# Kernel tuning notes

Hardware: AMD Instinct MI355X
Metric: run time of the kernel (lower is better)

The kernel has to match this reference:

```python
import jax, jax.numpy as jnp
import numpy as np

HEADS = 48
HEAD_DIM = 64
DIM = 3072
RANK = 128
TEXT_LEN = 226
VID_LEN = 1822
B = 1
LORA_W = 1.0
EPS = 1e-5


def setup_inputs() -> dict:
    key = jax.random.key(0)
    ks = jax.random.split(key, 24)
    s = 0.02  # weight init scale
    inp = {
        "hidden_states": jax.random.normal(ks[0], (B, VID_LEN, DIM), jnp.float32),
        "encoder_hidden_states": jax.random.normal(ks[1], (B, TEXT_LEN, DIM), jnp.float32),
        "rope_cos": jax.random.uniform(ks[2], (VID_LEN, HEAD_DIM), jnp.float32),
        "rope_sin": jax.random.uniform(ks[3], (VID_LEN, HEAD_DIM), jnp.float32),
        "Wq": jax.random.normal(ks[4], (DIM, DIM), jnp.float32) * s,
        "bq": jax.random.normal(ks[5], (DIM,), jnp.float32) * s,
        "Wk": jax.random.normal(ks[6], (DIM, DIM), jnp.float32) * s,
        "bk": jax.random.normal(ks[7], (DIM,), jnp.float32) * s,
        "Wv": jax.random.normal(ks[8], (DIM, DIM), jnp.float32) * s,
        "bv": jax.random.normal(ks[9], (DIM,), jnp.float32) * s,
        "Wo": jax.random.normal(ks[10], (DIM, DIM), jnp.float32) * s,
        "bo": jax.random.normal(ks[11], (DIM,), jnp.float32) * s,
        "lq_down": jax.random.normal(ks[12], (RANK, DIM), jnp.float32) / RANK,
        "lq_up": jax.random.normal(ks[13], (DIM, RANK), jnp.float32) * s,
        "lk_down": jax.random.normal(ks[14], (RANK, DIM), jnp.float32) / RANK,
        "lk_up": jax.random.normal(ks[15], (DIM, RANK), jnp.float32) * s,
        "lv_down": jax.random.normal(ks[16], (RANK, DIM), jnp.float32) / RANK,
        "lv_up": jax.random.normal(ks[17], (DIM, RANK), jnp.float32) * s,
        "lp_down": jax.random.normal(ks[18], (RANK, DIM), jnp.float32) / RANK,
        "lp_up": jax.random.normal(ks[19], (DIM, RANK), jnp.float32) * s,
        "gamma_q": jnp.ones((HEAD_DIM,), jnp.float32),
        "beta_q": jnp.zeros((HEAD_DIM,), jnp.float32),
        "gamma_k": jnp.ones((HEAD_DIM,), jnp.float32),
        "beta_k": jnp.zeros((HEAD_DIM,), jnp.float32),
    }
    return inp


def _lora(x, down, up):
    # x: [B,S,DIM]; down: [RANK,DIM]; up: [DIM,RANK]
    return (x @ down.T) @ up.T


def _layernorm(x, gamma, beta):
    mu = jnp.mean(x, axis=-1, keepdims=True)
    var = jnp.mean(jnp.square(x - mu), axis=-1, keepdims=True)
    return (x - mu) * jax.lax.rsqrt(var + EPS) * gamma + beta


def _apply_rope(x, cos, sin):
    # diffusers apply_rotary_emb, use_real=True, unbind_dim=-1
    # x: [B,H,S,D]; cos/sin: [S,D]
    xr = x.reshape(*x.shape[:-1], HEAD_DIM // 2, 2)
    x1, x2 = xr[..., 0], xr[..., 1]
    x_rot = jnp.stack([-x2, x1], axis=-1).reshape(x.shape)
    return x * cos + x_rot * sin


def reference(hidden_states, encoder_hidden_states, rope_cos, rope_sin,
              Wq, bq, Wk, bk, Wv, bv, Wo, bo,
              lq_down, lq_up, lk_down, lk_up, lv_down, lv_up, lp_down, lp_up,
              gamma_q, beta_q, gamma_k, beta_k):
    h = jnp.concatenate([encoder_hidden_states, hidden_states], axis=1)  # [B,S,DIM]
    S = h.shape[1]

    q = h @ Wq.T + bq + _lora(h, lq_down, lq_up) * LORA_W
    k = h @ Wk.T + bk + _lora(h, lk_down, lk_up) * LORA_W
    v = h @ Wv.T + bv + _lora(h, lv_down, lv_up) * LORA_W

    def split_heads(x):  # [B,S,DIM] -> [B,H,S,D]
        return x.reshape(B, S, HEADS, HEAD_DIM).transpose(0, 2, 1, 3)

    q, k, v = split_heads(q), split_heads(k), split_heads(v)
    q = _layernorm(q, gamma_q, beta_q)
    k = _layernorm(k, gamma_k, beta_k)

    # RoPE on video tokens only
    q = q.at[:, :, TEXT_LEN:].set(_apply_rope(q[:, :, TEXT_LEN:], rope_cos, rope_sin))
    k = k.at[:, :, TEXT_LEN:].set(_apply_rope(k[:, :, TEXT_LEN:], rope_cos, rope_sin))

    # scaled dot-product attention (no mask, no dropout)
    scale = 1.0 / np.sqrt(HEAD_DIM).astype(np.float32)
    scores = jnp.einsum("bhqd,bhkd->bhqk", q, k) * scale
    probs = jax.nn.softmax(scores, axis=-1)
    attn_out = jnp.einsum("bhqk,bhkd->bhqd", probs, v)

    out = attn_out.transpose(0, 2, 1, 3).reshape(B, S, DIM)
    out = out @ Wo.T + bo + _lora(out, lp_down, lp_up) * LORA_W

    enc_out = out[:, :TEXT_LEN, :]
    hid_out = out[:, TEXT_LEN:, :]
    return (hid_out, enc_out)
```

## Files before the change

kernel.cpp:

```cpp
#include <hip/hip_runtime.h>
#include <hip/hip_bf16.h>
#include <stdint.h>

#define S_TOT 2048
#define TEXT 226
#define VID 1822
#define DIM 3072
#define NH 48
#define HD 64

typedef __bf16 bf16x8 __attribute__((ext_vector_type(8)));
typedef __bf16 bf16x4 __attribute__((ext_vector_type(4)));
typedef float f32x4 __attribute__((ext_vector_type(4)));

#define AS1 __attribute__((address_space(1)))
#define AS3 __attribute__((address_space(3)))

__device__ __forceinline__ void g2l16(const void* g, void* l) {
    __builtin_amdgcn_global_load_lds((const AS1 uint32_t*)(uintptr_t)g,
                                     (AS3 uint32_t*)(uintptr_t)l, 16, 0, 0);
}

__device__ __forceinline__ f32x4 mfma16(bf16x4 a, bf16x4 b, f32x4 c) {
#if __has_builtin(__builtin_amdgcn_mfma_f32_16x16x16bf16_1k)
    typedef short s4 __attribute__((ext_vector_type(4)));
    union U { bf16x4 b; s4 s; };
    U ua, ub; ua.b = a; ub.b = b;
    return __builtin_amdgcn_mfma_f32_16x16x16bf16_1k(ua.s, ub.s, c, 0, 0, 0);
#else
    f32x4 d = c;
    asm volatile("v_mfma_f32_16x16x16_bf16 %0, %1, %2, %0"
                 : "+v"(d) : "v"(a), "v"(b));
    return d;
#endif
}

#define ARENA_N 47431680ull

struct NormArgs { const void* p[24]; };

__global__ __launch_bounds__(256)
void normalize_inputs(NormArgs a, __bf16* __restrict__ arena)
{
    static constexpr unsigned long long segStart[25] = {
        0ull, 694272ull, 6291456ull, 15728640ull, 25165824ull, 34603008ull,
        44040192ull, 44433408ull, 44826624ull, 45219840ull, 45613056ull,
        46006272ull, 46399488ull, 46792704ull, 47185920ull, 47302528ull,
        47419136ull, 47422208ull, 47425280ull, 47428352ull, 47431424ull,
        47431488ull, 47431552ull, 47431616ull, 47431680ull };
    static constexpr int segIn[24] = {
        1, 0, 4, 6, 8, 10, 12, 13, 14, 15, 16, 17, 18, 19, 2, 3,
        5, 7, 9, 11, 20, 21, 22, 23 };

    const uint32_t w0 = *(const uint32_t*)a.p[20];
    const bool f32in = (w0 == 0x3F800000u);

    const size_t i0 = ((size_t)blockIdx.x * 256 + threadIdx.x) * 8;
    if (i0 >= ARENA_N) return;
    int s = 0;
    while (i0 >= segStart[s + 1]) s++;
    const size_t off = i0 - segStart[s];

    if (f32in) {
        const float* src = (const float*)a.p[segIn[s]] + off;
        const float4 v0 = ((const float4*)src)[0];
        const float4 v1 = ((const float4*)src)[1];
        bf16x8 o;
        o[0] = (__bf16)v0.x; o[1] = (__bf16)v0.y; o[2] = (__bf16)v0.z; o[3] = (__bf16)v0.w;
        o[4] = (__bf16)v1.x; o[5] = (__bf16)v1.y; o[6] = (__bf16)v1.z; o[7] = (__bf16)v1.w;
        *(bf16x8*)(arena + i0) = o;
    } else {
        const __bf16* src = (const __bf16*)a.p[segIn[s]] + off;
        *(uint4*)(arena + i0) = *(const uint4*)src;
    }
}

__device__ __forceinline__ void mm_chunks(
    const __bf16* __restrict__ Ag, int lda, const __bf16* __restrict__ Bg, int ldb,
    int kbeg, int kend, f32x4 (&acc)[4][4], __bf16* As, __bf16* Bs,
    int wave, int srow, int l15, int quad, int wm, int wn)
{
    for (int k0 = kbeg; k0 < kend; k0 += 32) {
        __syncthreads();
#pragma unroll
        for (int i = 0; i < 2; i++) {
            const int blk = i * 4 + wave;
            const int r = blk * 16 + srow;
            g2l16(Ag + (size_t)r * lda + k0, &As[blk * 512]);
            g2l16(Bg + (size_t)r * ldb + k0, &Bs[blk * 512]);
        }
        __syncthreads();
        bf16x8 af[4], bfr[4];
#pragma unroll
        for (int i = 0; i < 4; i++)
            af[i] = *(const bf16x8*)&As[(wm + i * 16 + l15) * 32 + quad * 8];
#pragma unroll
        for (int j = 0; j < 4; j++)
            bfr[j] = *(const bf16x8*)&Bs[(wn + j * 16 + l15) * 32 + quad * 8];
#pragma unroll
        for (int i = 0; i < 4; i++)
#pragma unroll
            for (int j = 0; j < 4; j++)
                acc[i][j] = __builtin_amdgcn_mfma_f32_16x16x32_bf16(af[i], bfr[j], acc[i][j], 0, 0, 0);
    }
}

template<bool ATOMIC, bool FUSE2, bool TO_OUT>
__global__ __launch_bounds__(256)
void gemm_bt(const __bf16* __restrict__ A, int lda,
             const __bf16* __restrict__ B0, const __bf16* __restrict__ B1,
             const __bf16* __restrict__ B2, int ldb,
             const __bf16* __restrict__ bias0, const __bf16* __restrict__ bias1,
             const __bf16* __restrict__ bias2,
             const __bf16* __restrict__ A2, int lda2, int a2ColOff,
             const __bf16* __restrict__ U0, const __bf16* __restrict__ U1,
             const __bf16* __restrict__ U2, int ldu,
             float* __restrict__ C, int ldc,
             int K, int K2, int tilesPerGroup, int kChunk,
             void* __restrict__ dout, const void* __restrict__ probe)
{
    __shared__ __bf16 As[128 * 32];
    __shared__ __bf16 Bs[128 * 32];
    const int tid  = threadIdx.x;
    const int wave = tid >> 6;
    const int lane = tid & 63;
    const int l15  = lane & 15, quad = lane >> 4;
    const int bm = blockIdx.x, bn = blockIdx.y;
    const int group = bn / tilesPerGroup;
    const int nt    = bn - group * tilesPerGroup;
    const __bf16* B    = (group == 0) ? B0 : ((group == 1) ? B1 : B2);
    const __bf16* bias = (group == 0) ? bias0 : ((group == 1) ? bias1 : bias2);

    const int k0s = blockIdx.z * kChunk;
    int k0e = k0s + kChunk; if (k0e > K) k0e = K;

    const int srow = lane >> 2;
    const int schk = (lane & 3) * 8;
    const __bf16* Ag = A + (size_t)(bm * 128) * lda + schk;
    const __bf16* Bg = B + (size_t)(nt * 128) * ldb + schk;

    f32x4 acc[4][4] = {};
    const int wm = (wave & 1) * 64;
    const int wn = (wave >> 1) * 64;

    mm_chunks(Ag, lda, Bg, ldb, k0s, k0e, acc, As, Bs, wave, srow, l15, quad, wm, wn);

    if (FUSE2) {
        const __bf16* U = (group == 0) ? U0 : ((group == 1) ? U1 : U2);
        const __bf16* A2g = A2 + group * a2ColOff + (size_t)(bm * 128) * lda2 + schk;
        const __bf16* Ug  = U + (size_t)(nt * 128) * ldu + schk;
        mm_chunks(A2g, lda2, Ug, ldu, 0, K2, acc, As, Bs, wave, srow, l15, quad, wm, wn);
    }

    bool f32out = false;
    if (TO_OUT) f32out = (*(const uint32_t*)probe == 0x3F800000u);

#pragma unroll
    for (int i = 0; i < 4; i++) {
#pragma unroll
        for (int j = 0; j < 4; j++) {
            const int coll = wn + j * 16 + l15;
            const int col  = bn * 128 + coll;
            float bv = 0.f;
            if (bias) bv = (float)bias[nt * 128 + coll];
#pragma unroll
            for (int r = 0; r < 4; r++) {
                const int row = bm * 128 + wm + i * 16 + quad * 4 + r;
                float v = acc[i][j][r] + bv;
                if (TO_OUT) {
                    const size_t mrow = (row < TEXT) ? (size_t)(row + VID) : (size_t)(row - TEXT);
                    if (f32out) ((float*)dout)[mrow * DIM + col] = v;
                    else        ((__bf16*)dout)[mrow * DIM + col] = (__bf16)v;
                } else if (ATOMIC) {
                    atomicAdd(C + (size_t)row * ldc + col, v);
                } else {
                    C[(size_t)row * ldc + col] = v;
                }
            }
        }
    }
}

__global__ __launch_bounds__(256)
void ln_rope(const float* __restrict__ qkv,
             const __bf16* __restrict__ gq, const __bf16* __restrict__ bq,
             const __bf16* __restrict__ gk, const __bf16* __restrict__ bk,
             const __bf16* __restrict__ cosb, const __bf16* __restrict__ sinb,
             __bf16* __restrict__ qh, __bf16* __restrict__ kh)
{
    const int s = blockIdx.x;
    const int wave = threadIdx.x >> 6, lane = threadIdx.x & 63;
    for (int idx = wave; idx < 2 * NH; idx += 4) {
        const int mat  = idx / NH;
        const int head = idx - mat * NH;
        float x = qkv[(size_t)s * 9216 + mat * DIM + head * HD + lane];
        float mu = x;
        mu += __shfl_xor(mu, 1, 64);  mu += __shfl_xor(mu, 2, 64);
        mu += __shfl_xor(mu, 4, 64);  mu += __shfl_xor(mu, 8, 64);
        mu += __shfl_xor(mu, 16, 64); mu += __shfl_xor(mu, 32, 64);
        mu *= 0.015625f;
        float d = x - mu;
        float vv = d * d;
        vv += __shfl_xor(vv, 1, 64);  vv += __shfl_xor(vv, 2, 64);
        vv += __shfl_xor(vv, 4, 64);  vv += __shfl_xor(vv, 8, 64);
        vv += __shfl_xor(vv, 16, 64); vv += __shfl_xor(vv, 32, 64);
        vv *= 0.015625f;
        const float g = (float)(mat ? gk[lane] : gq[lane]);
        const float b = (float)(mat ? bk[lane] : bq[lane]);
        float y = d * rsqrtf(vv + 1e-5f) * g + b;
        if (s >= TEXT) {
            const int pos = s - TEXT;
            const float c  = (float)cosb[pos * HD + lane];
            const float sn = (float)sinb[pos * HD + lane];
            const float oth = __shfl_xor(y, 1, 64);
            const float rot = (lane & 1) ? oth : -oth;
            y = y * c + rot * sn;
        }
        __bf16* dst = mat ? kh : qh;
        dst[((size_t)head * S_TOT + s) * HD + lane] = (__bf16)y;
    }
}

__global__ __launch_bounds__(256)
void vtrans(const float* __restrict__ qkv, __bf16* __restrict__ vt)
{
    __shared__ float tile[64][65];
    const int h = blockIdx.x, sb = blockIdx.y;
    const int tid = threadIdx.x;
    const int r0 = tid >> 4;
    const int c0 = (tid & 15) * 4;
#pragma unroll
    for (int p = 0; p < 4; p++) {
        const int r = p * 16 + r0;
        const float4 v = *(const float4*)&qkv[((size_t)(sb * 64 + r)) * 9216 + 2 * DIM + h * HD + c0];
        tile[r][c0 + 0] = v.x; tile[r][c0 + 1] = v.y;
        tile[r][c0 + 2] = v.z; tile[r][c0 + 3] = v.w;
    }
    __syncthreads();
#pragma unroll
    for (int p = 0; p < 4; p++) {
        const int d = p * 16 + r0;
        __bf16 o[4];
#pragma unroll
        for (int e = 0; e < 4; e++) o[e] = (__bf16)tile[c0 + e][d];
        *(uint2*)&vt[((size_t)(h * HD + d)) * S_TOT + sb * 64 + c0] = *(const uint2*)o;
    }
}

#define KS_LD 72
#define VS_LD 136

__global__ __launch_bounds__(256)
void flash_attn(const __bf16* __restrict__ qh, const __bf16* __restrict__ kh,
                const __bf16* __restrict__ vt, __bf16* __restrict__ outp)
{
    __shared__ __bf16 Ks[128 * KS_LD];
    __shared__ __bf16 Vs[64 * VS_LD];
    const int qb = blockIdx.x, h = blockIdx.y;
    const int tid = threadIdx.x, wave = tid >> 6, lane = tid & 63;
    const int l15 = lane & 15, quad = lane >> 4;

    bf16x8 qf[2][2];
#pragma unroll
    for (int t = 0; t < 2; t++)
#pragma unroll
        for (int ks = 0; ks < 2; ks++) {
            const __bf16* p = qh + ((size_t)(h * S_TOT + qb * 128 + wave * 32 + t * 16 + l15)) * HD
                                 + ks * 32 + quad * 8;
            bf16x8 v = *(const bf16x8*)p;
#pragma unroll
            for (int e = 0; e < 8; e++) v[e] = (__bf16)((float)v[e] * 0.125f);
            qf[t][ks] = v;
        }

    f32x4 of[2][4] = {};
    float m_i[2] = {-1e30f, -1e30f};
    float l_i[2] = {0.f, 0.f};
    const float L2E = 1.44269504f;

    for (int kb = 0; kb < S_TOT / 128; kb++) {
        bf16x8 kr[4], vr[4];
#pragma unroll
        for (int p = 0; p < 4; p++) {
            const int id = p * 256 + tid;
            const int krow = id >> 3, kc = (id & 7) * 8;
            kr[p] = *(const bf16x8*)(kh + ((size_t)(h * S_TOT + kb * 128 + krow)) * HD + kc);
            const int vrow = id >> 4, vc = (id & 15) * 8;
            vr[p] = *(const bf16x8*)(vt + ((size_t)(h * HD + vrow)) * S_TOT + kb * 128 + vc);
        }
        __syncthreads();
#pragma unroll
        for (int p = 0; p < 4; p++) {
            const int id = p * 256 + tid;
            const int krow = id >> 3, kc = (id & 7) * 8;
            *(bf16x8*)&Ks[krow * KS_LD + kc] = kr[p];
            const int vrow = id >> 4, vc = (id & 15) * 8;
            *(bf16x8*)&Vs[vrow * VS_LD + vc] = vr[p];
        }
        __syncthreads();

        f32x4 sf[2][8];
#pragma unroll
        for (int n = 0; n < 8; n++) {
            const bf16x8 k0 = *(const bf16x8*)&Ks[(n * 16 + l15) * KS_LD + quad * 8];
            const bf16x8 k1 = *(const bf16x8*)&Ks[(n * 16 + l15) * KS_LD + 32 + quad * 8];
#pragma unroll
            for (int t = 0; t < 2; t++) {
                f32x4 z = {0.f, 0.f, 0.f, 0.f};
                z = __builtin_amdgcn_mfma_f32_16x16x32_bf16(k0, qf[t][0], z, 0, 0, 0);
                sf[t][n] = __builtin_amdgcn_mfma_f32_16x16x32_bf16(k1, qf[t][1], z, 0, 0, 0);
            }
        }

        float alpha_l[2];
#pragma unroll
        for (int t = 0; t < 2; t++) {
            float mx = sf[t][0][0];
#pragma unroll
            for (int n = 0; n < 8; n++)
#pragma unroll
                for (int r = 0; r < 4; r++) mx = fmaxf(mx, sf[t][n][r]);
            mx = fmaxf(mx, __shfl_xor(mx, 16, 64));
            mx = fmaxf(mx, __shfl_xor(mx, 32, 64));
            const float mnew = fmaxf(m_i[t], mx);
            alpha_l[t] = __builtin_amdgcn_exp2f((m_i[t] - mnew) * L2E);
            m_i[t] = mnew;
            float rs = 0.f;
#pragma unroll
            for (int n = 0; n < 8; n++)
#pragma unroll
                for (int r = 0; r < 4; r++) {
                    const float pv = __builtin_amdgcn_exp2f((sf[t][n][r] - mnew) * L2E);
                    sf[t][n][r] = pv;
                    rs += pv;
                }
            rs += __shfl_xor(rs, 16, 64);
            rs += __shfl_xor(rs, 32, 64);
            l_i[t] = l_i[t] * alpha_l[t] + rs;
        }

        bf16x4 pf[2][8];
#pragma unroll
        for (int t = 0; t < 2; t++)
#pragma unroll
            for (int kk = 0; kk < 8; kk++) {
                bf16x4 o;
                o[0] = (__bf16)sf[t][kk][0]; o[1] = (__bf16)sf[t][kk][1];
                o[2] = (__bf16)sf[t][kk][2]; o[3] = (__bf16)sf[t][kk][3];
                pf[t][kk] = o;
            }

#pragma unroll
        for (int t = 0; t < 2; t++)
#pragma unroll
            for (int r = 0; r < 4; r++) {
                const float a_r = __shfl(alpha_l[t], quad * 4 + r, 16);
#pragma unroll
                for (int j = 0; j < 4; j++) of[t][j][r] *= a_r;
            }

#pragma unroll
        for (int kk = 0; kk < 8; kk++) {
#pragma unroll
            for (int j = 0; j < 4; j++) {
                const bf16x4 vf = *(const bf16x4*)&Vs[(j * 16 + l15) * VS_LD + kk * 16 + quad * 4];
                of[0][j] = mfma16(pf[0][kk], vf, of[0][j]);
                of[1][j] = mfma16(pf[1][kk], vf, of[1][j]);
            }
        }
    }

#pragma unroll
    for (int t = 0; t < 2; t++)
#pragma unroll
        for (int r = 0; r < 4; r++) {
            const float lr = __shfl(l_i[t], quad * 4 + r, 16);
            const float inv = 1.f / lr;
            const int row = qb * 128 + wave * 32 + t * 16 + quad * 4 + r;
#pragma unroll
            for (int j = 0; j < 4; j++)
                outp[(size_t)row * DIM + h * HD + j * 16 + l15] = (__bf16)(of[t][j][r] * inv);
        }
}

__global__ __launch_bounds__(256)
void f32_to_bf16(const float* __restrict__ src, __bf16* __restrict__ dst, int n4)
{
    const int i = blockIdx.x * blockDim.x + threadIdx.x;
    if (i < n4) {
        const float4 v = ((const float4*)src)[i];
        __bf16 o[4] = {(__bf16)v.x, (__bf16)v.y, (__bf16)v.z, (__bf16)v.w};
        ((uint2*)dst)[i] = *(const uint2*)o;
    }
}

extern "C" void kernel_launch(void* const* d_in, const int* in_sizes, int n_in,
                              void* d_out, int out_size, void* d_ws, size_t ws_size,
                              hipStream_t stream)
{
    char* ws = (char*)d_ws;
    __bf16* arena = (__bf16*)ws;

    const __bf16* h     = arena + 0;
    const __bf16* Wq    = arena + 6291456;
    const __bf16* Wk    = arena + 15728640;
    const __bf16* Wv    = arena + 25165824;
    const __bf16* Wo    = arena + 34603008;
    const __bf16* lqd   = arena + 44040192;
    const __bf16* lqu   = arena + 44433408;
    const __bf16* lkd   = arena + 44826624;
    const __bf16* lku   = arena + 45219840;
    const __bf16* lvd   = arena + 45613056;
    const __bf16* lvu   = arena + 46006272;
    const __bf16* lpd   = arena + 46399488;
    const __bf16* lpu   = arena + 46792704;
    const __bf16* ropec = arena + 47185920;
    const __bf16* ropes = arena + 47302528;
    const __bf16* bq    = arena + 47419136;
    const __bf16* bk    = arena + 47422208;
    const __bf16* bv    = arena + 47425280;
    const __bf16* bo    = arena + 47428352;
    const __bf16* gq    = arena + 47431424;
    const __bf16* btq   = arena + 47431488;
    const __bf16* gk    = arena + 47431552;
    const __bf16* btk   = arena + 47431616;

    float*  qkvf = (float*)(ws + 94863360);
    float*  t32  = (float*)(ws + 170360832);
    __bf16* t16  = (__bf16*)(ws + 174555136);
    __bf16* qh   = (__bf16*)(ws + 176652288);
    __bf16* kh   = (__bf16*)(ws + 189235200);
    __bf16* vt   = (__bf16*)(ws + 201818112);
    __bf16* attn = (__bf16*)(ws + 0);

    NormArgs na;
    for (int i = 0; i < 24; i++) na.p[i] = d_in[i];
    normalize_inputs<<<(unsigned)((ARENA_N / 8 + 255) / 256), 256, 0, stream>>>(na, arena);

    hipMemsetAsync(t32, 0, (size_t)2048 * 512 * 4, stream);

    gemm_bt<true, false, false><<<dim3(16, 3, 4), 256, 0, stream>>>(
        h, DIM, lqd, lkd, lvd, DIM, nullptr, nullptr, nullptr,
        nullptr, 0, 0, nullptr, nullptr, nullptr, 0,
        t32, 512, DIM, 0, 1, 768, nullptr, nullptr);
    f32_to_bf16<<<(2048 * 512 / 4 + 255) / 256, 256, 0, stream>>>(t32, t16, 2048 * 512 / 4);

    gemm_bt<false, true, false><<<dim3(16, 72, 1), 256, 0, stream>>>(
        h, DIM, Wq, Wk, Wv, DIM, bq, bk, bv,
        t16, 512, 128, lqu, lku, lvu, 128,
        qkvf, 9216, DIM, 128, 24, DIM, nullptr, nullptr);

    ln_rope<<<2048, 256, 0, stream>>>(qkvf, gq, btq, gk, btk, ropec, ropes, qh, kh);
    vtrans<<<dim3(48, 32), 256, 0, stream>>>(qkvf, vt);
    flash_attn<<<dim3(16, 48), 256, 0, stream>>>(qh, kh, vt, attn);

    gemm_bt<true, false, false><<<dim3(16, 1, 4), 256, 0, stream>>>(
        attn, DIM, lpd, lpd, lpd, DIM, nullptr, nullptr, nullptr,
        nullptr, 0, 0, nullptr, nullptr, nullptr, 0,
        t32 + 384, 512, DIM, 0, 1, 768, nullptr, nullptr);
    f32_to_bf16<<<(2048 * 512 / 4 + 255) / 256, 256, 0, stream>>>(t32, t16, 2048 * 512 / 4);

    gemm_bt<false, true, true><<<dim3(16, 24, 1), 256, 0, stream>>>(
        attn, DIM, Wo, Wo, Wo, DIM, bo, bo, bo,
        t16 + 384, 512, 0, lpu, lpu, lpu, 128,
        nullptr, 0, DIM, 128, 24, DIM, d_out, d_in[20]);
}
```

Measured before the change: 716.3 us.

## Fuse QK layernorm, RoPE and V transpose into QKV GEMM epilogue; swizzle LDS

The QKV projection GEMM epilogue now applies per-head layernorm and RoPE to Q and K and writes them directly in head-major bf16 layout. It also writes V transposed, which removes the fp32 QKV intermediate buffer and the separate ln_rope and vtrans kernels. Separately, the LDS tile layout is XOR-style swizzled on the global-to-LDS write and the fragment reads to reduce bank conflicts in all GEMMs. The cost is heavier epilogue register and shuffle work, plus uncoalesced-ish 8-byte stores for the transposed V.

Measured after the change: 737.3 us. 1.03x slower.

```diff
diff --git a/kernel.cpp b/kernel.cpp
--- a/kernel.cpp
+++ b/kernel.cpp
@@ -78,7 +78,7 @@
 __device__ __forceinline__ void mm_chunks(
     const __bf16* __restrict__ Ag, int lda, const __bf16* __restrict__ Bg, int ldb,
     int kbeg, int kend, f32x4 (&acc)[4][4], __bf16* As, __bf16* Bs,
-    int wave, int srow, int l15, int quad, int wm, int wn)
+    int wave, int srow, int schk, int rdoff, int l15, int wm, int wn)
 {
     for (int k0 = kbeg; k0 < kend; k0 += 32) {
         __syncthreads();
@@ -86,17 +86,17 @@
         for (int i = 0; i < 2; i++) {
             const int blk = i * 4 + wave;
             const int r = blk * 16 + srow;
-            g2l16(Ag + (size_t)r * lda + k0, &As[blk * 512]);
-            g2l16(Bg + (size_t)r * ldb + k0, &Bs[blk * 512]);
+            g2l16(Ag + (size_t)r * lda + k0 + schk, &As[blk * 512]);
+            g2l16(Bg + (size_t)r * ldb + k0 + schk, &Bs[blk * 512]);
         }
         __syncthreads();
         bf16x8 af[4], bfr[4];
 #pragma unroll
         for (int i = 0; i < 4; i++)
-            af[i] = *(const bf16x8*)&As[(wm + i * 16 + l15) * 32 + quad * 8];
+            af[i] = *(const bf16x8*)&As[(wm + i * 16 + l15) * 32 + rdoff];
 #pragma unroll
         for (int j = 0; j < 4; j++)
-            bfr[j] = *(const bf16x8*)&Bs[(wn + j * 16 + l15) * 32 + quad * 8];
+            bfr[j] = *(const bf16x8*)&Bs[(wn + j * 16 + l15) * 32 + rdoff];
 #pragma unroll
         for (int i = 0; i < 4; i++)
 #pragma unroll
@@ -105,7 +105,14 @@
     }
 }
 
-template<bool ATOMIC, bool FUSE2, bool TO_OUT>
+struct EpiArgs {
+    __bf16* qh; __bf16* kh; __bf16* vt;
+    const __bf16* ropec; const __bf16* ropes;
+    const __bf16* gq; const __bf16* btq; const __bf16* gk; const __bf16* btk;
+    void* dout; const void* probe;
+};
+
+template<int MODE, bool ATOMIC, bool FUSE2>
 __global__ __launch_bounds__(256)
 void gemm_bt(const __bf16* __restrict__ A, int lda,
              const __bf16* __restrict__ B0, const __bf16* __restrict__ B1,
@@ -116,8 +123,7 @@
              const __bf16* __restrict__ U0, const __bf16* __restrict__ U1,
              const __bf16* __restrict__ U2, int ldu,
              float* __restrict__ C, int ldc,
-             int K, int K2, int tilesPerGroup, int kChunk,
-             void* __restrict__ dout, const void* __restrict__ probe)
+             int K, int K2, int tilesPerGroup, int kChunk, EpiArgs ea)
 {
     __shared__ __bf16 As[128 * 32];
     __shared__ __bf16 Bs[128 * 32];
@@ -134,26 +140,93 @@
     const int k0s = blockIdx.z * kChunk;
     int k0e = k0s + kChunk; if (k0e > K) k0e = K;
 
-    const int srow = lane >> 2;
-    const int schk = (lane & 3) * 8;
-    const __bf16* Ag = A + (size_t)(bm * 128) * lda + schk;
-    const __bf16* Bg = B + (size_t)(nt * 128) * ldb + schk;
+    const int srow  = lane >> 2;
+    const int schk  = ((((lane & 3) - (lane >> 3)) & 3)) * 8;
+    const int rdoff = ((quad + (l15 >> 1)) & 3) * 8;
+    const __bf16* Ag = A + (size_t)(bm * 128) * lda;
+    const __bf16* Bg = B + (size_t)(nt * 128) * ldb;
 
     f32x4 acc[4][4] = {};
     const int wm = (wave & 1) * 64;
     const int wn = (wave >> 1) * 64;
 
-    mm_chunks(Ag, lda, Bg, ldb, k0s, k0e, acc, As, Bs, wave, srow, l15, quad, wm, wn);
+    mm_chunks(Ag, lda, Bg, ldb, k0s, k0e, acc, As, Bs, wave, srow, schk, rdoff, l15, wm, wn);
 
     if (FUSE2) {
         const __bf16* U = (group == 0) ? U0 : ((group == 1) ? U1 : U2);
-        const __bf16* A2g = A2 + group * a2ColOff + (size_t)(bm * 128) * lda2 + schk;
-        const __bf16* Ug  = U + (size_t)(nt * 128) * ldu + schk;
-        mm_chunks(A2g, lda2, Ug, ldu, 0, K2, acc, As, Bs, wave, srow, l15, quad, wm, wn);
+        const __bf16* A2g = A2 + group * a2ColOff + (size_t)(bm * 128) * lda2;
+        const __bf16* Ug  = U + (size_t)(nt * 128) * ldu;
+        mm_chunks(A2g, lda2, Ug, ldu, 0, K2, acc, As, Bs, wave, srow, schk, rdoff, l15, wm, wn);
+    }
+
+    if (MODE == 2) {
+        const int head = nt * 2 + (wn >> 6);
+        float bv[4];
+#pragma unroll
+        for (int j = 0; j < 4; j++)
+            bv[j] = bias ? (float)bias[nt * 128 + wn + j * 16 + l15] : 0.f;
+
+        if (group == 2) {
+#pragma unroll
+            for (int i = 0; i < 4; i++) {
+                const int rowb = bm * 128 + wm + i * 16 + quad * 4;
+#pragma unroll
+                for (int j = 0; j < 4; j++) {
+                    const int d = j * 16 + l15;
+                    __bf16 o[4];
+#pragma unroll
+                    for (int r = 0; r < 4; r++) o[r] = (__bf16)(acc[i][j][r] + bv[j]);
+                    *(uint2*)&ea.vt[((size_t)(head * HD + d)) * S_TOT + rowb] = *(const uint2*)o;
+                }
+            }
+        } else {
+            const __bf16* gam = group ? ea.gk : ea.gq;
+            const __bf16* bet = group ? ea.btk : ea.btq;
+            __bf16* dst = group ? ea.kh : ea.qh;
+            float g[4], bb[4];
+#pragma unroll
+            for (int j = 0; j < 4; j++) {
+                g[j]  = (float)gam[j * 16 + l15];
+                bb[j] = (float)bet[j * 16 + l15];
+            }
+#pragma unroll
+            for (int i = 0; i < 4; i++) {
+#pragma unroll
+                for (int r = 0; r < 4; r++) {
+                    const int row = bm * 128 + wm + i * 16 + quad * 4 + r;
+                    float x[4];
+#pragma unroll
+                    for (int j = 0; j < 4; j++) x[j] = acc[i][j][r] + bv[j];
+                    float s = x[0] + x[1] + x[2] + x[3];
+                    s += __shfl_xor(s, 1, 64); s += __shfl_xor(s, 2, 64);
+                    s += __shfl_xor(s, 4, 64); s += __shfl_xor(s, 8, 64);
+                    const float mu = s * 0.015625f;
+                    float vv = 0.f;
+#pragma unroll
+                    for (int j = 0; j < 4; j++) { const float dd = x[j] - mu; vv += dd * dd; }
+                    vv += __shfl_xor(vv, 1, 64); vv += __shfl_xor(vv, 2, 64);
+                    vv += __shfl_xor(vv, 4, 64); vv += __shfl_xor(vv, 8, 64);
+                    const float rin = rsqrtf(vv * 0.015625f + 1e-5f);
+                    const int pos = (row >= TEXT) ? (row - TEXT) : 0;
+#pragma unroll
+                    for (int j = 0; j < 4; j++) {
+                        float y = (x[j] - mu) * rin * g[j] + bb[j];
+                        const float c  = (float)ea.ropec[pos * HD + j * 16 + l15];
+                        const float sn = (float)ea.ropes[pos * HD + j * 16 + l15];
+                        const float oth = __shfl_xor(y, 1, 64);
+                        const float rot = (l15 & 1) ? oth : -oth;
+                        const float yr = y * c + rot * sn;
+                        y = (row >= TEXT) ? yr : y;
+                        dst[((size_t)(head * S_TOT + row)) * HD + j * 16 + l15] = (__bf16)y;
+                    }
+                }
+            }
+        }
+        return;
     }
 
     bool f32out = false;
-    if (TO_OUT) f32out = (*(const uint32_t*)probe == 0x3F800000u);
+    if (MODE == 1) f32out = (*(const uint32_t*)ea.probe == 0x3F800000u);
 
 #pragma unroll
     for (int i = 0; i < 4; i++) {
@@ -167,10 +240,10 @@
             for (int r = 0; r < 4; r++) {
                 const int row = bm * 128 + wm + i * 16 + quad * 4 + r;
                 float v = acc[i][j][r] + bv;
-                if (TO_OUT) {
+                if (MODE == 1) {
                     const size_t mrow = (row < TEXT) ? (size_t)(row + VID) : (size_t)(row - TEXT);
-                    if (f32out) ((float*)dout)[mrow * DIM + col] = v;
-                    else        ((__bf16*)dout)[mrow * DIM + col] = (__bf16)v;
+                    if (f32out) ((float*)ea.dout)[mrow * DIM + col] = v;
+                    else        ((__bf16*)ea.dout)[mrow * DIM + col] = (__bf16)v;
                 } else if (ATOMIC) {
                     atomicAdd(C + (size_t)row * ldc + col, v);
                 } else {
@@ -178,72 +251,6 @@
                 }
             }
         }
-    }
-}
-
-__global__ __launch_bounds__(256)
-void ln_rope(const float* __restrict__ qkv,
-             const __bf16* __restrict__ gq, const __bf16* __restrict__ bq,
-             const __bf16* __restrict__ gk, const __bf16* __restrict__ bk,
-             const __bf16* __restrict__ cosb, const __bf16* __restrict__ sinb,
-             __bf16* __restrict__ qh, __bf16* __restrict__ kh)
-{
-    const int s = blockIdx.x;
-    const int wave = threadIdx.x >> 6, lane = threadIdx.x & 63;
-    for (int idx = wave; idx < 2 * NH; idx += 4) {
-        const int mat  = idx / NH;
-        const int head = idx - mat * NH;
-        float x = qkv[(size_t)s * 9216 + mat * DIM + head * HD + lane];
-        float mu = x;
-        mu += __shfl_xor(mu, 1, 64);  mu += __shfl_xor(mu, 2, 64);
-        mu += __shfl_xor(mu, 4, 64);  mu += __shfl_xor(mu, 8, 64);
-        mu += __shfl_xor(mu, 16, 64); mu += __shfl_xor(mu, 32, 64);
-        mu *= 0.015625f;
-        float d = x - mu;
-        float vv = d * d;
-        vv += __shfl_xor(vv, 1, 64);  vv += __shfl_xor(vv, 2, 64);
-        vv += __shfl_xor(vv, 4, 64);  vv += __shfl_xor(vv, 8, 64);
-        vv += __shfl_xor(vv, 16, 64); vv += __shfl_xor(vv, 32, 64);
-        vv *= 0.015625f;
-        const float g = (float)(mat ? gk[lane] : gq[lane]);
-        const float b = (float)(mat ? bk[lane] : bq[lane]);
-        float y = d * rsqrtf(vv + 1e-5f) * g + b;
-        if (s >= TEXT) {
-            const int pos = s - TEXT;
-            const float c  = (float)cosb[pos * HD + lane];
-            const float sn = (float)sinb[pos * HD + lane];
-            const float oth = __shfl_xor(y, 1, 64);
-            const float rot = (lane & 1) ? oth : -oth;
-            y = y * c + rot * sn;
-        }
-        __bf16* dst = mat ? kh : qh;
-        dst[((size_t)head * S_TOT + s) * HD + lane] = (__bf16)y;
-    }
-}
-
-__global__ __launch_bounds__(256)
-void vtrans(const float* __restrict__ qkv, __bf16* __restrict__ vt)
-{
-    __shared__ float tile[64][65];
-    const int h = blockIdx.x, sb = blockIdx.y;
-    const int tid = threadIdx.x;
-    const int r0 = tid >> 4;
-    const int c0 = (tid & 15) * 4;
-#pragma unroll
-    for (int p = 0; p < 4; p++) {
-        const int r = p * 16 + r0;
-        const float4 v = *(const float4*)&qkv[((size_t)(sb * 64 + r)) * 9216 + 2 * DIM + h * HD + c0];
-        tile[r][c0 + 0] = v.x; tile[r][c0 + 1] = v.y;
-        tile[r][c0 + 2] = v.z; tile[r][c0 + 3] = v.w;
-    }
-    __syncthreads();
-#pragma unroll
-    for (int p = 0; p < 4; p++) {
-        const int d = p * 16 + r0;
-        __bf16 o[4];
-#pragma unroll
-        for (int e = 0; e < 4; e++) o[e] = (__bf16)tile[c0 + e][d];
-        *(uint2*)&vt[((size_t)(h * HD + d)) * S_TOT + sb * 64 + c0] = *(const uint2*)o;
     }
 }
 
@@ -425,7 +432,6 @@
     const __bf16* gk    = arena + 47431552;
     const __bf16* btk   = arena + 47431616;
 
-    float*  qkvf = (float*)(ws + 94863360);
     float*  t32  = (float*)(ws + 170360832);
     __bf16* t16  = (__bf16*)(ws + 174555136);
     __bf16* qh   = (__bf16*)(ws + 176652288);
@@ -433,35 +439,38 @@
     __bf16* vt   = (__bf16*)(ws + 201818112);
     __bf16* attn = (__bf16*)(ws + 0);
 
+    EpiArgs eaNone = {};
+    EpiArgs eaQKV = { qh, kh, vt, ropec, ropes, gq, btq, gk, btk, nullptr, nullptr };
+    EpiArgs eaOut = {};
+    eaOut.dout = d_out; eaOut.probe = d_in[20];
+
     NormArgs na;
     for (int i = 0; i < 24; i++) na.p[i] = d_in[i];
     normalize_inputs<<<(unsigned)((ARENA_N / 8 + 255) / 256), 256, 0, stream>>>(na, arena);
 
     hipMemsetAsync(t32, 0, (size_t)2048 * 512 * 4, stream);
 
-    gemm_bt<true, false, false><<<dim3(16, 3, 4), 256, 0, stream>>>(
+    gemm_bt<0, true, false><<<dim3(16, 3, 4), 256, 0, stream>>>(
         h, DIM, lqd, lkd, lvd, DIM, nullptr, nullptr, nullptr,
         nullptr, 0, 0, nullptr, nullptr, nullptr, 0,
-        t32, 512, DIM, 0, 1, 768, nullptr, nullptr);
+        t32, 512, DIM, 0, 1, 768, eaNone);
     f32_to_bf16<<<(2048 * 512 / 4 + 255) / 256, 256, 0, stream>>>(t32, t16, 2048 * 512 / 4);
 
-    gemm_bt<false, true, false><<<dim3(16, 72, 1), 256, 0, stream>>>(
+    gemm_bt<2, false, true><<<dim3(16, 72, 1), 256, 0, stream>>>(
         h, DIM, Wq, Wk, Wv, DIM, bq, bk, bv,
         t16, 512, 128, lqu, lku, lvu, 128,
-        qkvf, 9216, DIM, 128, 24, DIM, nullptr, nullptr);
-
-    ln_rope<<<2048, 256, 0, stream>>>(qkvf, gq, btq, gk, btk, ropec, ropes, qh, kh);
-    vtrans<<<dim3(48, 32), 256, 0, stream>>>(qkvf, vt);
+        nullptr, 0, DIM, 128, 24, DIM, eaQKV);
+
     flash_attn<<<dim3(16, 48), 256, 0, stream>>>(qh, kh, vt, attn);
 
-    gemm_bt<true, false, false><<<dim3(16, 1, 4), 256, 0, stream>>>(
+    gemm_bt<0, true, false><<<dim3(16, 1, 4), 256, 0, stream>>>(
         attn, DIM, lpd, lpd, lpd, DIM, nullptr, nullptr, nullptr,
         nullptr, 0, 0, nullptr, nullptr, nullptr, 0,
-        t32 + 384, 512, DIM, 0, 1, 768, nullptr, nullptr);
+        t32 + 384, 512, DIM, 0, 1, 768, eaNone);
     f32_to_bf16<<<(2048 * 512 / 4 + 255) / 256, 256, 0, stream>>>(t32, t16, 2048 * 512 / 4);
 
-    gemm_bt<false, true, true><<<dim3(16, 24, 1), 256, 0, stream>>>(
+    gemm_bt<1, false, true><<<dim3(16, 24, 1), 256, 0, stream>>>(
         attn, DIM, Wo, Wo, Wo, DIM, bo, bo, bo,
         t16 + 384, 512, 0, lpu, lpu, lpu, 128,
-        nullptr, 0, DIM, 128, 24, DIM, d_out, d_in[20]);
-}
+        nullptr, 0, DIM, 128, 24, DIM, eaOut);
+}
```
